# Performance work log

Hardware: AMD Instinct MI355X
Metric: run time of the kernel (lower is better)

Reference implementation:

```python
import jax, jax.numpy as jnp
import numpy as np

N = 1_000_000   # half-edges
C = 64          # in_channels == out_channels (out = empty_like(x))


def setup_inputs() -> dict:
    key = jax.random.key(0)
    k1, k2, k3, k4, k5, k6 = jax.random.split(key, 6)
    x = jax.random.normal(k1, (N, C), dtype=jnp.float32)
    next_idx = jax.random.randint(k2, (N,), 0, N, dtype=jnp.int32)
    twin_idx = jax.random.randint(k3, (N,), 0, N, dtype=jnp.int32)
    has_twin = jax.random.randint(k4, (N,), 0, 2, dtype=jnp.int32).astype(jnp.bool_)
    # nn.Linear(2C, C): weight [C, 2C], bias [C]; kaiming-uniform-ish init scale
    bound = 1.0 / np.sqrt(2 * C)
    W = jax.random.uniform(k5, (C, 2 * C), dtype=jnp.float32, minval=-bound, maxval=bound)
    b = jax.random.uniform(k6, (C,), dtype=jnp.float32, minval=-bound, maxval=bound)
    return {"x": x, "next_idx": next_idx, "twin_idx": twin_idx,
            "has_twin": has_twin, "W": W, "b": b}


def reference(x, next_idx, twin_idx, has_twin, W, b):
    # per-half-edge gather of next/twin vertex features (twin zero-filled if absent)
    next_f = x[next_idx]                                   # [N, C]
    twin_f = jnp.where(has_twin[:, None], x[twin_idx], 0.0)  # [N, C]
    neighbor = jnp.concatenate([next_f, twin_f], axis=-1)  # [N, 2C]
    out = neighbor @ W.T + b                               # [N, C]
    return jax.nn.relu(out)
```

## Files before the change

### kernel.cpp

```cpp
#include <hip/hip_runtime.h>
#include <hip/hip_bf16.h>
#include <stdint.h>

typedef __attribute__((ext_vector_type(4))) float f32x4;
typedef __attribute__((ext_vector_type(8))) __bf16 bf16x8;

#define NROWS 1000000

__device__ __forceinline__ bf16x8 cvt8(f32x4 a, f32x4 b) {
    bf16x8 r;
    r[0] = (__bf16)a[0]; r[1] = (__bf16)a[1];
    r[2] = (__bf16)a[2]; r[3] = (__bf16)a[3];
    r[4] = (__bf16)b[0]; r[5] = (__bf16)b[1];
    r[6] = (__bf16)b[2]; r[7] = (__bf16)b[3];
    return r;
}

__global__ void heconv_mfma(const float* __restrict__ x,
                            const int* __restrict__ nidx,
                            const int* __restrict__ tidx,
                            const int* __restrict__ ht,
                            const float* __restrict__ W,
                            const float* __restrict__ bias,
                            float* __restrict__ out)
{
    const int lane = threadIdx.x & 63;
    const int wave = threadIdx.x >> 6;
    const int lrow = lane & 15;
    const int lkg  = lane >> 4;

    bf16x8 wfrag[4][4];
#pragma unroll
    for (int ct = 0; ct < 4; ++ct) {
        const float* wrow = W + (ct * 16 + lrow) * 128 + lkg * 8;
#pragma unroll
        for (int ks = 0; ks < 4; ++ks) {
            f32x4 w0 = *(const f32x4*)(wrow + ks * 32);
            f32x4 w1 = *(const f32x4*)(wrow + ks * 32 + 4);
            wfrag[ct][ks] = cvt8(w0, w1);
        }
    }
    f32x4 bfrag[4];
#pragma unroll
    for (int ct = 0; ct < 4; ++ct)
        bfrag[ct] = *(const f32x4*)(bias + ct * 16 + lkg * 4);

    const int nGroups = NROWS / 16;
    const int gstride = gridDim.x * 4;
    for (int g = blockIdx.x * 4 + wave; g < nGroups; g += gstride) {
        const int r  = g * 16 + lrow;
        const int ni = nidx[r];
        const int ti = tidx[r];
        const bool tw = ht[r] != 0;

        bf16x8 xf[4];
        {
            const float* nrow = x + (size_t)ni * 64 + lkg * 8;
            f32x4 n0 = *(const f32x4*)(nrow);
            f32x4 n1 = *(const f32x4*)(nrow + 4);
            f32x4 n2 = *(const f32x4*)(nrow + 32);
            f32x4 n3 = *(const f32x4*)(nrow + 36);
            xf[0] = cvt8(n0, n1);
            xf[1] = cvt8(n2, n3);
        }
        if (tw) {
            const float* trow = x + (size_t)ti * 64 + lkg * 8;
            f32x4 t0 = *(const f32x4*)(trow);
            f32x4 t1 = *(const f32x4*)(trow + 4);
            f32x4 t2 = *(const f32x4*)(trow + 32);
            f32x4 t3 = *(const f32x4*)(trow + 36);
            xf[2] = cvt8(t0, t1);
            xf[3] = cvt8(t2, t3);
        } else {
            bf16x8 z = { (__bf16)0.f, (__bf16)0.f, (__bf16)0.f, (__bf16)0.f,
                         (__bf16)0.f, (__bf16)0.f, (__bf16)0.f, (__bf16)0.f };
            xf[2] = z;
            xf[3] = z;
        }

#pragma unroll
        for (int ct = 0; ct < 4; ++ct) {
            f32x4 acc = bfrag[ct];
#pragma unroll
            for (int ks = 0; ks < 4; ++ks)
                acc = __builtin_amdgcn_mfma_f32_16x16x32_bf16(wfrag[ct][ks], xf[ks], acc, 0, 0, 0);
            f32x4 o;
            o[0] = fmaxf(acc[0], 0.f);
            o[1] = fmaxf(acc[1], 0.f);
            o[2] = fmaxf(acc[2], 0.f);
            o[3] = fmaxf(acc[3], 0.f);
            *(f32x4*)(out + (size_t)r * 64 + ct * 16 + lkg * 4) = o;
        }
    }
}

extern "C" void kernel_launch(void* const* d_in, const int* in_sizes, int n_in,
                              void* d_out, int out_size, void* d_ws, size_t ws_size,
                              hipStream_t stream) {
    const float* x    = (const float*)d_in[0];
    const int*   ni   = (const int*)d_in[1];
    const int*   ti   = (const int*)d_in[2];
    const int*   ht   = (const int*)d_in[3];
    const float* W    = (const float*)d_in[4];
    const float* bias = (const float*)d_in[5];
    float*       out  = (float*)d_out;

    heconv_mfma<<<2048, 256, 0, stream>>>(x, ni, ti, ht, W, bias, out);
}
```

Measured before the change: 157.0 us.

## Software-pipeline index loads and process two row groups per iteration

Each wave now handles two 16-row groups per loop iteration, issuing all gather loads for both groups up front. It also prefetches the next iteration's indices while the current gathers are in flight, which raises memory-level parallelism on the latency-bound random gathers. Twin rows are now always loaded and masked with a select rather than skipped by a branch, which adds gather traffic for rows without a twin. Output writes use nontemporal stores. Register pressure rises from the extra in-flight values and may reduce occupancy.

```diff
diff --git a/kernel.cpp b/kernel.cpp
--- a/kernel.cpp
+++ b/kernel.cpp
@@ -46,51 +46,104 @@
         bfrag[ct] = *(const f32x4*)(bias + ct * 16 + lkg * 4);
 
     const int nGroups = NROWS / 16;
-    const int gstride = gridDim.x * 4;
-    for (int g = blockIdx.x * 4 + wave; g < nGroups; g += gstride) {
-        const int r  = g * 16 + lrow;
-        const int ni = nidx[r];
-        const int ti = tidx[r];
-        const bool tw = ht[r] != 0;
+    const int gs  = gridDim.x * 4;
+    const int wid = blockIdx.x * 4 + wave;
 
-        bf16x8 xf[4];
-        {
-            const float* nrow = x + (size_t)ni * 64 + lkg * 8;
-            f32x4 n0 = *(const f32x4*)(nrow);
-            f32x4 n1 = *(const f32x4*)(nrow + 4);
-            f32x4 n2 = *(const f32x4*)(nrow + 32);
-            f32x4 n3 = *(const f32x4*)(nrow + 36);
-            xf[0] = cvt8(n0, n1);
-            xf[1] = cvt8(n2, n3);
+    int niA = 0, tiA = 0, htA = 0, niB = 0, tiB = 0, htB = 0;
+    if (wid < nGroups) {
+        int r = wid * 16 + lrow;
+        niA = nidx[r]; tiA = tidx[r]; htA = ht[r];
+        if (wid + gs < nGroups) {
+            int r2 = (wid + gs) * 16 + lrow;
+            niB = nidx[r2]; tiB = tidx[r2]; htB = ht[r2];
         }
-        if (tw) {
-            const float* trow = x + (size_t)ti * 64 + lkg * 8;
-            f32x4 t0 = *(const f32x4*)(trow);
-            f32x4 t1 = *(const f32x4*)(trow + 4);
-            f32x4 t2 = *(const f32x4*)(trow + 32);
-            f32x4 t3 = *(const f32x4*)(trow + 36);
-            xf[2] = cvt8(t0, t1);
-            xf[3] = cvt8(t2, t3);
-        } else {
-            bf16x8 z = { (__bf16)0.f, (__bf16)0.f, (__bf16)0.f, (__bf16)0.f,
-                         (__bf16)0.f, (__bf16)0.f, (__bf16)0.f, (__bf16)0.f };
-            xf[2] = z;
-            xf[3] = z;
+    }
+
+    for (int g = wid; g < nGroups; g += 2 * gs) {
+        const bool hasB = (g + gs) < nGroups;
+
+        const float* pnA = x + (size_t)niA * 64 + lkg * 8;
+        const float* ptA = x + (size_t)tiA * 64 + lkg * 8;
+        f32x4 nA0 = *(const f32x4*)(pnA);
+        f32x4 nA1 = *(const f32x4*)(pnA + 4);
+        f32x4 nA2 = *(const f32x4*)(pnA + 32);
+        f32x4 nA3 = *(const f32x4*)(pnA + 36);
+        f32x4 tA0 = *(const f32x4*)(ptA);
+        f32x4 tA1 = *(const f32x4*)(ptA + 4);
+        f32x4 tA2 = *(const f32x4*)(ptA + 32);
+        f32x4 tA3 = *(const f32x4*)(ptA + 36);
+
+        f32x4 nB0, nB1, nB2, nB3, tB0, tB1, tB2, tB3;
+        if (hasB) {
+            const float* pnB = x + (size_t)niB * 64 + lkg * 8;
+            const float* ptB = x + (size_t)tiB * 64 + lkg * 8;
+            nB0 = *(const f32x4*)(pnB);
+            nB1 = *(const f32x4*)(pnB + 4);
+            nB2 = *(const f32x4*)(pnB + 32);
+            nB3 = *(const f32x4*)(pnB + 36);
+            tB0 = *(const f32x4*)(ptB);
+            tB1 = *(const f32x4*)(ptB + 4);
+            tB2 = *(const f32x4*)(ptB + 32);
+            tB3 = *(const f32x4*)(ptB + 36);
         }
 
+        const int gn = g + 2 * gs;
+        int niA2 = 0, tiA2 = 0, htA2 = 0, niB2 = 0, tiB2 = 0, htB2 = 0;
+        if (gn < nGroups) {
+            int r = gn * 16 + lrow;
+            niA2 = nidx[r]; tiA2 = tidx[r]; htA2 = ht[r];
+            if (gn + gs < nGroups) {
+                int r2 = (gn + gs) * 16 + lrow;
+                niB2 = nidx[r2]; tiB2 = tidx[r2]; htB2 = ht[r2];
+            }
+        }
+
+        {
+            const f32x4 z = {0.f, 0.f, 0.f, 0.f};
+            f32x4 m0 = htA ? tA0 : z, m1 = htA ? tA1 : z;
+            f32x4 m2 = htA ? tA2 : z, m3 = htA ? tA3 : z;
+            bf16x8 xf[4] = { cvt8(nA0, nA1), cvt8(nA2, nA3),
+                             cvt8(m0, m1),   cvt8(m2, m3) };
+            const int r = g * 16 + lrow;
 #pragma unroll
-        for (int ct = 0; ct < 4; ++ct) {
-            f32x4 acc = bfrag[ct];
+            for (int ct = 0; ct < 4; ++ct) {
+                f32x4 acc = bfrag[ct];
 #pragma unroll
-            for (int ks = 0; ks < 4; ++ks)
-                acc = __builtin_amdgcn_mfma_f32_16x16x32_bf16(wfrag[ct][ks], xf[ks], acc, 0, 0, 0);
-            f32x4 o;
-            o[0] = fmaxf(acc[0], 0.f);
-            o[1] = fmaxf(acc[1], 0.f);
-            o[2] = fmaxf(acc[2], 0.f);
-            o[3] = fmaxf(acc[3], 0.f);
-            *(f32x4*)(out + (size_t)r * 64 + ct * 16 + lkg * 4) = o;
+                for (int ks = 0; ks < 4; ++ks)
+                    acc = __builtin_amdgcn_mfma_f32_16x16x32_bf16(wfrag[ct][ks], xf[ks], acc, 0, 0, 0);
+                f32x4 o;
+                o[0] = fmaxf(acc[0], 0.f);
+                o[1] = fmaxf(acc[1], 0.f);
+                o[2] = fmaxf(acc[2], 0.f);
+                o[3] = fmaxf(acc[3], 0.f);
+                __builtin_nontemporal_store(o, (f32x4*)(out + (size_t)r * 64 + ct * 16 + lkg * 4));
+            }
         }
+
+        if (hasB) {
+            const f32x4 z = {0.f, 0.f, 0.f, 0.f};
+            f32x4 m0 = htB ? tB0 : z, m1 = htB ? tB1 : z;
+            f32x4 m2 = htB ? tB2 : z, m3 = htB ? tB3 : z;
+            bf16x8 xf[4] = { cvt8(nB0, nB1), cvt8(nB2, nB3),
+                             cvt8(m0, m1),   cvt8(m2, m3) };
+            const int r = (g + gs) * 16 + lrow;
+#pragma unroll
+            for (int ct = 0; ct < 4; ++ct) {
+                f32x4 acc = bfrag[ct];
+#pragma unroll
+                for (int ks = 0; ks < 4; ++ks)
+                    acc = __builtin_amdgcn_mfma_f32_16x16x32_bf16(wfrag[ct][ks], xf[ks], acc, 0, 0, 0);
+                f32x4 o;
+                o[0] = fmaxf(acc[0], 0.f);
+                o[1] = fmaxf(acc[1], 0.f);
+                o[2] = fmaxf(acc[2], 0.f);
+                o[3] = fmaxf(acc[3], 0.f);
+                __builtin_nontemporal_store(o, (f32x4*)(out + (size_t)r * 64 + ct * 16 + lkg * 4));
+            }
+        }
+
+        niA = niA2; tiA = tiA2; htA = htA2;
+        niB = niB2; tiB = tiB2; htB = htB2;
     }
 }
 
```

After: 272.5 us. 1.74x slower.
